# Kernel optimization log

Measured on AMD Instinct MI355X. Metric: run time of the kernel, lower is better.

Reference implementation:

```python
import jax, jax.numpy as jnp
import numpy as np


def setup_inputs() -> dict:
    key = jax.random.key(0)
    k1, k2, k3 = jax.random.split(key, 3)
    B, C, H, W = 8, 128, 256, 256
    K = 7
    x = jax.random.normal(k1, (B, C, H, W), dtype=jnp.float32)
    # PyTorch Conv2d default init: U(-b, b), b = 1/sqrt(fan_in), fan_in = 1*K*K
    bound = 1.0 / np.sqrt(K * K)
    conv_w = jax.random.uniform(k2, (1, 1, K, K), minval=-bound, maxval=bound, dtype=jnp.float32)
    conv_b = jax.random.uniform(k3, (1,), minval=-bound, maxval=bound, dtype=jnp.float32)
    return {"input": x, "conv_w": conv_w, "conv_b": conv_b}


def reference(input, conv_w, conv_b):
    # ChannelPool: max over channel dim, keep dim -> [B,1,H,W]
    pooled = jnp.max(input, axis=1, keepdims=True)
    # 7x7 conv (1->1), stride 1, pad 3 (SAME for odd kernel)
    conv = jax.lax.conv_general_dilated(
        pooled, conv_w,
        window_strides=(1, 1), padding=[(3, 3), (3, 3)],
        dimension_numbers=("NCHW", "OIHW", "NCHW"),
    ) + conv_b[None, :, None, None]
    attn = jax.nn.sigmoid(conv)  # [B,1,H,W]
    return input * attn  # broadcast over channels
```

## Files before the change

### kernel.cpp

```cpp
#include <hip/hip_runtime.h>

#define Bc 8
#define Cc 128
#define Hc 256
#define Wc 256
#define HWc (Hc * Wc)
#define CHWc (Cc * HWc)

typedef float floatx4 __attribute__((ext_vector_type(4)));

__global__ void __launch_bounds__(256) channel_max_kernel(const float* __restrict__ in,
                                                          float* __restrict__ pooled) {
    int tid = blockIdx.x * blockDim.x + threadIdx.x;
    int e = tid << 2;
    int b = e / HWc;
    int s = e - b * HWc;
    const floatx4* base = (const floatx4*)(in + (size_t)b * CHWc + s);
    const int cstride = HWc / 4;

    floatx4 m0 = base[0];
    floatx4 m1 = base[(size_t)cstride];
#pragma unroll 4
    for (int c = 2; c < Cc; c += 2) {
        floatx4 v0 = base[(size_t)c * cstride];
        floatx4 v1 = base[(size_t)(c + 1) * cstride];
        m0.x = fmaxf(m0.x, v0.x); m0.y = fmaxf(m0.y, v0.y);
        m0.z = fmaxf(m0.z, v0.z); m0.w = fmaxf(m0.w, v0.w);
        m1.x = fmaxf(m1.x, v1.x); m1.y = fmaxf(m1.y, v1.y);
        m1.z = fmaxf(m1.z, v1.z); m1.w = fmaxf(m1.w, v1.w);
    }
    floatx4 m;
    m.x = fmaxf(m0.x, m1.x); m.y = fmaxf(m0.y, m1.y);
    m.z = fmaxf(m0.z, m1.z); m.w = fmaxf(m0.w, m1.w);
    ((floatx4*)pooled)[tid] = m;
}

__global__ void __launch_bounds__(256) conv_sigmoid_kernel(const float* __restrict__ pooled,
                                                           const float* __restrict__ wgt,
                                                           const float* __restrict__ bias,
                                                           float* __restrict__ attn) {
    __shared__ float wsm[49];
    if (threadIdx.x < 49) wsm[threadIdx.x] = wgt[threadIdx.x];
    __syncthreads();

    int tid = blockIdx.x * blockDim.x + threadIdx.x;
    int b = tid / HWc;
    int s = tid - b * HWc;
    int h = s >> 8;
    int w = s & (Wc - 1);
    const float* p = pooled + b * HWc;

    float acc = bias[0];
#pragma unroll
    for (int i = 0; i < 7; ++i) {
        int hh = h - 3 + i;
        if ((unsigned)hh < (unsigned)Hc) {
            const float* row = p + hh * Wc;
#pragma unroll
            for (int j = 0; j < 7; ++j) {
                int ww = w - 3 + j;
                if ((unsigned)ww < (unsigned)Wc) {
                    acc = fmaf(row[ww], wsm[i * 7 + j], acc);
                }
            }
        }
    }
    attn[tid] = 1.0f / (1.0f + expf(-acc));
}

__global__ void __launch_bounds__(256) mul_kernel(const float* __restrict__ in,
                                                  const float* __restrict__ attn,
                                                  float* __restrict__ out) {
    unsigned rb = gridDim.x - 1u - blockIdx.x;
    unsigned tid = rb * blockDim.x + threadIdx.x;
    unsigned e = tid << 2;
    unsigned b = e / (unsigned)CHWc;
    unsigned s = e & (HWc - 1);
    floatx4 v = *(const floatx4*)(in + e);
    floatx4 a = *(const floatx4*)(attn + b * HWc + s);
    v.x *= a.x;
    v.y *= a.y;
    v.z *= a.z;
    v.w *= a.w;
    __builtin_nontemporal_store(v, (floatx4*)(out + e));
}

extern "C" void kernel_launch(void* const* d_in, const int* in_sizes, int n_in,
                              void* d_out, int out_size, void* d_ws, size_t ws_size,
                              hipStream_t stream) {
    const float* input  = (const float*)d_in[0];
    const float* conv_w = (const float*)d_in[1];
    const float* conv_b = (const float*)d_in[2];
    float* out = (float*)d_out;

    float* pooled = (float*)d_ws;
    float* attn   = pooled + (size_t)Bc * HWc;

    channel_max_kernel<<<(Bc * HWc / 4) / 256, 256, 0, stream>>>(input, pooled);

    conv_sigmoid_kernel<<<(Bc * HWc) / 256, 256, 0, stream>>>(pooled, conv_w, conv_b, attn);

    mul_kernel<<<(Bc * CHWc / 4) / 256, 256, 0, stream>>>(input, attn, out);
}
```

Baseline: 487.5 us.

## Fuse conv+sigmoid into the broadcast multiply kernel with channel-chunked blocks

Merges the 7x7 conv/sigmoid kernel and the multiply kernel into one. Each thread computes attention for 4 adjacent pixels and applies it across a chunk of 32 channels, with 4 chunks per pixel group. This drops the attn buffer write and read and one kernel launch. In exchange the conv is recomputed 4 times, once per chunk, and each thread's global reads are more serialized.

```diff
diff --git a/kernel.cpp b/kernel.cpp
--- a/kernel.cpp
+++ b/kernel.cpp
@@ -6,6 +6,9 @@
 #define Wc 256
 #define HWc (Hc * Wc)
 #define CHWc (Cc * HWc)
+
+#define NCHUNK 4
+#define CPB (Cc / NCHUNK)
 
 typedef float floatx4 __attribute__((ext_vector_type(4)));
 
@@ -35,54 +38,64 @@
     ((floatx4*)pooled)[tid] = m;
 }
 
-__global__ void __launch_bounds__(256) conv_sigmoid_kernel(const float* __restrict__ pooled,
-                                                           const float* __restrict__ wgt,
-                                                           const float* __restrict__ bias,
-                                                           float* __restrict__ attn) {
+__global__ void __launch_bounds__(256) conv_mul_kernel(const float* __restrict__ in,
+                                                       const float* __restrict__ pooled,
+                                                       const float* __restrict__ wgt,
+                                                       const float* __restrict__ bias,
+                                                       float* __restrict__ out) {
     __shared__ float wsm[49];
     if (threadIdx.x < 49) wsm[threadIdx.x] = wgt[threadIdx.x];
     __syncthreads();
 
-    int tid = blockIdx.x * blockDim.x + threadIdx.x;
-    int b = tid / HWc;
-    int s = tid - b * HWc;
-    int h = s >> 8;
-    int w = s & (Wc - 1);
+    unsigned bid = blockIdx.x;
+    unsigned chunk = bid & (NCHUNK - 1);
+    unsigned pgBlocks = gridDim.x / NCHUNK;
+    unsigned pgb = pgBlocks - 1u - (bid >> 2);
+    unsigned t = pgb * blockDim.x + threadIdx.x;
+    unsigned e = t << 2;
+    unsigned b = e >> 16;
+    unsigned s = e & (HWc - 1);
+    int h = (int)(s >> 8);
+    int w0 = (int)(s & (Wc - 1));
+
     const float* p = pooled + b * HWc;
-
-    float acc = bias[0];
+    float attn[4];
 #pragma unroll
-    for (int i = 0; i < 7; ++i) {
-        int hh = h - 3 + i;
-        if ((unsigned)hh < (unsigned)Hc) {
-            const float* row = p + hh * Wc;
+    for (int k = 0; k < 4; ++k) {
+        float acc = bias[0];
+        int w = w0 + k;
 #pragma unroll
-            for (int j = 0; j < 7; ++j) {
-                int ww = w - 3 + j;
-                if ((unsigned)ww < (unsigned)Wc) {
-                    acc = fmaf(row[ww], wsm[i * 7 + j], acc);
+        for (int i = 0; i < 7; ++i) {
+            int hh = h - 3 + i;
+            if ((unsigned)hh < (unsigned)Hc) {
+                const float* row = p + hh * Wc;
+#pragma unroll
+                for (int j = 0; j < 7; ++j) {
+                    int ww = w - 3 + j;
+                    if ((unsigned)ww < (unsigned)Wc) {
+                        acc = fmaf(row[ww], wsm[i * 7 + j], acc);
+                    }
                 }
             }
         }
+        attn[k] = 1.0f / (1.0f + expf(-acc));
     }
-    attn[tid] = 1.0f / (1.0f + expf(-acc));
-}
+    floatx4 a;
+    a.x = attn[0]; a.y = attn[1]; a.z = attn[2]; a.w = attn[3];
 
-__global__ void __launch_bounds__(256) mul_kernel(const float* __restrict__ in,
-                                                  const float* __restrict__ attn,
-                                                  float* __restrict__ out) {
-    unsigned rb = gridDim.x - 1u - blockIdx.x;
-    unsigned tid = rb * blockDim.x + threadIdx.x;
-    unsigned e = tid << 2;
-    unsigned b = e / (unsigned)CHWc;
-    unsigned s = e & (HWc - 1);
-    floatx4 v = *(const floatx4*)(in + e);
-    floatx4 a = *(const floatx4*)(attn + b * HWc + s);
-    v.x *= a.x;
-    v.y *= a.y;
-    v.z *= a.z;
-    v.w *= a.w;
-    __builtin_nontemporal_store(v, (floatx4*)(out + e));
+    const size_t base = (size_t)b * CHWc + (size_t)chunk * CPB * HWc + s;
+    const floatx4* ip = (const floatx4*)(in + base);
+    float* op = out + base;
+    const int cstride = HWc / 4;
+#pragma unroll 4
+    for (int c = 0; c < CPB; ++c) {
+        floatx4 v = ip[(size_t)c * cstride];
+        v.x *= a.x;
+        v.y *= a.y;
+        v.z *= a.z;
+        v.w *= a.w;
+        __builtin_nontemporal_store(v, (floatx4*)(op) + (size_t)c * cstride);
+    }
 }
 
 extern "C" void kernel_launch(void* const* d_in, const int* in_sizes, int n_in,
@@ -94,11 +107,9 @@
     float* out = (float*)d_out;
 
     float* pooled = (float*)d_ws;
-    float* attn   = pooled + (size_t)Bc * HWc;
 
     channel_max_kernel<<<(Bc * HWc / 4) / 256, 256, 0, stream>>>(input, pooled);
 
-    conv_sigmoid_kernel<<<(Bc * HWc) / 256, 256, 0, stream>>>(pooled, conv_w, conv_b, attn);
-
-    mul_kernel<<<(Bc * CHWc / 4) / 256, 256, 0, stream>>>(input, attn, out);
+    conv_mul_kernel<<<NCHUNK * (Bc * HWc / 4) / 256, 256, 0, stream>>>(
+        input, pooled, conv_w, conv_b, out);
 }
```

Measured after the change: 524.2 us. +7.5%, slower.
